# Kernel tuning notes

Measured on AMD Instinct MI355X. Metric: run time of the kernel, lower is better.

## Reference

```python
import jax, jax.numpy as jnp
import numpy as np

SEQ_LEN = 16384
IN_DIM = 2048
STATE_DIM = 2048


def setup_inputs() -> dict:
    key = jax.random.key(0)
    k_xs, k_lam, k_win, k_c, k_d = jax.random.split(key, 5)
    xs = jax.random.normal(k_xs, (SEQ_LEN, IN_DIM), dtype=jnp.float32)
    # diagonal state-transition values in (0, 1) for stability
    lam = jax.random.uniform(k_lam, (STATE_DIM,), dtype=jnp.float32)
    w_in = jax.random.normal(k_win, (STATE_DIM, IN_DIM), dtype=jnp.float32) / np.float32(np.sqrt(IN_DIM))
    c_out = jax.random.normal(k_c, (IN_DIM, STATE_DIM), dtype=jnp.float32) / np.float32(np.sqrt(STATE_DIM))
    d_skip = jax.random.normal(k_d, (IN_DIM,), dtype=jnp.float32)
    return {"xs": xs, "lam": lam, "w_in": w_in, "c_out": c_out, "d_skip": d_skip}


def _ssm_cell(a, b):
    # Faithful replication of BaseSSMLayer.ssm_cell (including its use of
    # matrix_pow_i * matrix_pow_i for the first component, exactly as in source).
    matrix_pow_i, bx_i = a
    matrix_pow_j, bx_j = b
    return (matrix_pow_i * matrix_pow_i, matrix_pow_j * bx_i + bx_j)


def reference(xs, lam, w_in, c_out, d_skip):
    seq_len = xs.shape[0]
    # discretize: broadcast diagonal lambda over the sequence -> [L, N]
    lambda_elements = jnp.broadcast_to(lam, (seq_len, lam.shape[0]))
    # preprocess_inputs: vmap(w_in @ x) == xs @ w_in.T  -> [L, N]
    w_in_xs = jnp.einsum('li,ni->ln', xs, w_in)
    _, hs = jax.lax.associative_scan(_ssm_cell, (lambda_elements, w_in_xs))
    # postprocess: y_t = C h_t + D * x_t  -> [L, in_dim]
    return jnp.einsum('ln,on->lo', hs, c_out) + xs * d_skip
```

## Files before the change

### kernel.cpp

```cpp
#include <hip/hip_runtime.h>

#define SEQ   16384
#define DIM   2048
#define CHUNK 128
#define NCHUNK (SEQ / CHUNK)

typedef __attribute__((ext_vector_type(8))) short  short8;
typedef __attribute__((ext_vector_type(4))) short  short4v;
typedef __attribute__((ext_vector_type(4))) float  floatx4;

static __device__ __forceinline__ float bf2f(short s) {
    return __uint_as_float(((unsigned)(unsigned short)s) << 16);
}
static __device__ __forceinline__ short f2bf(float f) {
    unsigned u = __float_as_uint(f);
    u += 0x7fff + ((u >> 16) & 1);
    return (short)(u >> 16);
}

__global__ void cast_kernel(const float* __restrict__ in, short* __restrict__ out, int n4) {
    int i = blockIdx.x * blockDim.x + threadIdx.x;
    if (i >= n4) return;
    float4 v = ((const float4*)in)[i];
    short4v s;
    s.x = f2bf(v.x); s.y = f2bf(v.y); s.z = f2bf(v.z); s.w = f2bf(v.w);
    ((short4v*)out)[i] = s;
}


#define BAR   __builtin_amdgcn_s_barrier()
#define PRIO1 __builtin_amdgcn_s_setprio(1)
#define PRIO0 __builtin_amdgcn_s_setprio(0)
#define VMC6  asm volatile("s_waitcnt vmcnt(6)" ::: "memory")
#define VMC0  asm volatile("s_waitcnt vmcnt(0)" ::: "memory")

#define STAGE_A(b, h, t) do { \
    const short* _s = Abase + (size_t)(h) * 128 * K + (size_t)(t) * 64; \
    __builtin_amdgcn_global_load_lds(_s + gOff0, &As[b][h][c0 * 8], 16, 0, 0); \
    __builtin_amdgcn_global_load_lds(_s + gOff1, &As[b][h][c1 * 8], 16, 0, 0); \
} while (0)
#define STAGE_B(b, h, t) do { \
    const short* _s = Bbase + (size_t)(h) * 128 * K + (size_t)(t) * 64; \
    __builtin_amdgcn_global_load_lds(_s + gOff0, &Bs[b][h][c0 * 8], 16, 0, 0); \
    __builtin_amdgcn_global_load_lds(_s + gOff1, &Bs[b][h][c1 * 8], 16, 0, 0); \
} while (0)

#define LDA(b, mh) \
    _Pragma("unroll") \
    for (int mi = 0; mi < 4; mi++) { \
        _Pragma("unroll") \
        for (int ks = 0; ks < 2; ks++) \
            aV[mi][ks] = *(const short8*)&As[b][mh][(arow + mi * 16) * 64 + \
                                                    ((((ks << 2) | quad) ^ sx) << 3)]; \
    }
#define LDB(dst, b, nh) \
    _Pragma("unroll") \
    for (int ni = 0; ni < 2; ni++) { \
        _Pragma("unroll") \
        for (int ks = 0; ks < 2; ks++) \
            dst[ni][ks] = *(const short8*)&Bs[b][nh][(brow + ni * 16) * 64 + \
                                                     ((((ks << 2) | quad) ^ sx) << 3)]; \
    }
#define MMA(mh, nh, bR) \
    _Pragma("unroll") \
    for (int mi = 0; mi < 4; mi++) { \
        _Pragma("unroll") \
        for (int ni = 0; ni < 2; ni++) { \
            acc[mh][nh][mi][ni] = __builtin_amdgcn_mfma_f32_16x16x32_bf16( \
                aV[mi][0], bR[ni][0], acc[mh][nh][mi][ni], 0, 0, 0); \
            acc[mh][nh][mi][ni] = __builtin_amdgcn_mfma_f32_16x16x32_bf16( \
                aV[mi][1], bR[ni][1], acc[mh][nh][mi][ni], 0, 0, 0); \
        } \
    }

template<int FUSE>
__global__ __launch_bounds__(512, 2)
void gemm_bt(const short* __restrict__ A, const short* __restrict__ B,
             short* __restrict__ Cbf, float* __restrict__ Cf,
             const float* __restrict__ xs, const float* __restrict__ dskip)
{
    constexpr int K  = DIM;
    constexpr int NT = K / 64;

    __shared__ alignas(16) short As[2][2][128 * 64];
    __shared__ alignas(16) short Bs[2][2][128 * 64];

    const int tid = threadIdx.x;
    const int m0  = blockIdx.y * 256;
    const int n0  = blockIdx.x * 256;

    const int lane = tid & 63;
    const int wv   = tid >> 6;
    const int wrow = wv >> 2;
    const int wcol = wv & 3;
    const int l16  = lane & 15;
    const int quad = lane >> 4;
    const int sx   = l16 & 7;
    const int arow = wrow * 64 + l16;
    const int brow = wcol * 32 + l16;

    const int c0 = tid, c1 = tid + 512;
    const int r0 = c0 >> 3, r1 = c1 >> 3;
    const size_t gOff0 = (size_t)r0 * K + (size_t)((((c0 & 7) ^ (r0 & 7))) * 8);
    const size_t gOff1 = (size_t)r1 * K + (size_t)((((c1 & 7) ^ (r1 & 7))) * 8);
    const short* Abase = A + (size_t)m0 * K;
    const short* Bbase = B + (size_t)n0 * K;

    short8  aV[4][2], bA[2][2], bB[2][2];
    floatx4 acc[2][2][4][2] = {};

    STAGE_A(0, 0, 0); STAGE_B(0, 0, 0); STAGE_B(0, 1, 0); STAGE_A(0, 1, 0);
    STAGE_A(1, 0, 1); STAGE_B(1, 0, 1); STAGE_B(1, 1, 1);
    VMC6;
    BAR;

    for (int i = 0; i < NT / 2; ++i) {
        const int t1 = 2 * i + 1;
        const int t2 = (2 * i + 2) & (NT - 1);
        const int t3 = (2 * i + 3) & (NT - 1);

        LDA(0, 0); LDB(bA, 0, 0); STAGE_A(1, 1, t1);
        PRIO1; MMA(0, 0, bA); PRIO0;
        BAR;
        LDB(bB, 0, 1); STAGE_A(0, 0, t2);
        PRIO1; MMA(0, 1, bB); PRIO0;
        BAR;
        LDA(0, 1); STAGE_B(0, 0, t2);
        PRIO1; MMA(1, 0, bA); PRIO0;
        BAR;
        STAGE_B(0, 1, t2);
        PRIO1; MMA(1, 1, bB); PRIO0;
        VMC6;
        BAR;
        LDA(1, 0); LDB(bA, 1, 0); STAGE_A(0, 1, t2);
        PRIO1; MMA(0, 0, bA); PRIO0;
        BAR;
        LDB(bB, 1, 1); STAGE_A(1, 0, t3);
        PRIO1; MMA(0, 1, bB); PRIO0;
        BAR;
        LDA(1, 1); STAGE_B(1, 0, t3);
        PRIO1; MMA(1, 0, bA); PRIO0;
        BAR;
        STAGE_B(1, 1, t3);
        PRIO1; MMA(1, 1, bB); PRIO0;
        VMC6;
        BAR;
    }
    VMC0;

    if (FUSE == 0) {
        #pragma unroll
        for (int mh = 0; mh < 2; mh++)
        #pragma unroll
        for (int mi = 0; mi < 4; mi++) {
            const int rb = m0 + wrow * 64 + mh * 128 + mi * 16 + quad * 4;
            #pragma unroll
            for (int nh = 0; nh < 2; nh++)
            #pragma unroll
            for (int ni = 0; ni < 2; ni++) {
                const int cc = n0 + wcol * 32 + nh * 128 + ni * 16 + l16;
                #pragma unroll
                for (int r = 0; r < 4; r++)
                    Cbf[(size_t)(rb + r) * DIM + cc] = f2bf(acc[mh][nh][mi][ni][r]);
            }
        }
    } else {
        float dsk[2][2];
        #pragma unroll
        for (int nh = 0; nh < 2; nh++)
        #pragma unroll
        for (int ni = 0; ni < 2; ni++)
            dsk[nh][ni] = dskip[n0 + wcol * 32 + nh * 128 + ni * 16 + l16];
        #pragma unroll
        for (int mh = 0; mh < 2; mh++)
        #pragma unroll
        for (int mi = 0; mi < 4; mi++) {
            const int rb = m0 + wrow * 64 + mh * 128 + mi * 16 + quad * 4;
            #pragma unroll
            for (int nh = 0; nh < 2; nh++)
            #pragma unroll
            for (int ni = 0; ni < 2; ni++) {
                const int cc = n0 + wcol * 32 + nh * 128 + ni * 16 + l16;
                #pragma unroll
                for (int r = 0; r < 4; r++) {
                    size_t idx = (size_t)(rb + r) * DIM + cc;
                    Cf[idx] = acc[mh][nh][mi][ni][r] + xs[idx] * dsk[nh][ni];
                }
            }
        }
    }
}

__global__ void scan_pass1(const short* __restrict__ bx, const float* __restrict__ lam,
                           float* __restrict__ blockLast)
{
    int q     = blockIdx.x * 256 + threadIdx.x;
    int n     = q * 4;
    int chunk = blockIdx.y;
    float4 lm = *(const float4*)&lam[n];
    const uint2* p = (const uint2*)(bx + (size_t)chunk * CHUNK * DIM) + q;
    float h0 = 0.f, h1 = 0.f, h2 = 0.f, h3 = 0.f;
    #pragma unroll 16
    for (int i = 0; i < CHUNK; i++) {
        uint2 v = p[(size_t)i * (DIM / 4)];
        h0 = fmaf(lm.x, h0, bf2f((short)(v.x & 0xffffu)));
        h1 = fmaf(lm.y, h1, bf2f((short)(v.x >> 16)));
        h2 = fmaf(lm.z, h2, bf2f((short)(v.y & 0xffffu)));
        h3 = fmaf(lm.w, h3, bf2f((short)(v.y >> 16)));
    }
    float4 o; o.x = h0; o.y = h1; o.z = h2; o.w = h3;
    *(float4*)&blockLast[(size_t)chunk * DIM + n] = o;
}

__global__ void scan_pass2(float* __restrict__ blockLast, const float* __restrict__ lam)
{
    int q = blockIdx.x * 256 + threadIdx.x;
    int n = q * 4;
    float4 lm = *(const float4*)&lam[n];
    float p0 = lm.x, p1 = lm.y, p2 = lm.z, p3 = lm.w;
    #pragma unroll
    for (int i = 0; i < 7; i++) { p0 *= p0; p1 *= p1; p2 *= p2; p3 *= p3; }
    float c0 = 0.f, c1 = 0.f, c2 = 0.f, c3 = 0.f;
    for (int c = 0; c < NCHUNK; c++) {
        float4* qp = (float4*)&blockLast[(size_t)c * DIM + n];
        float4 t = *qp;
        float4 w; w.x = c0; w.y = c1; w.z = c2; w.w = c3;
        *qp = w;
        c0 = fmaf(p0, c0, t.x);
        c1 = fmaf(p1, c1, t.y);
        c2 = fmaf(p2, c2, t.z);
        c3 = fmaf(p3, c3, t.w);
    }
}

__global__ void scan_pass3(short* __restrict__ bxh, const float* __restrict__ lam,
                           const float* __restrict__ carry)
{
    int q     = blockIdx.x * 256 + threadIdx.x;
    int n     = q * 4;
    int chunk = blockIdx.y;
    float4 lm = *(const float4*)&lam[n];
    float4 cv = *(const float4*)&carry[(size_t)chunk * DIM + n];
    float h0 = cv.x, h1 = cv.y, h2 = cv.z, h3 = cv.w;
    uint2* p = (uint2*)(bxh + (size_t)chunk * CHUNK * DIM) + q;
    #pragma unroll 16
    for (int i = 0; i < CHUNK; i++) {
        uint2 v = p[(size_t)i * (DIM / 4)];
        h0 = fmaf(lm.x, h0, bf2f((short)(v.x & 0xffffu)));
        h1 = fmaf(lm.y, h1, bf2f((short)(v.x >> 16)));
        h2 = fmaf(lm.z, h2, bf2f((short)(v.y & 0xffffu)));
        h3 = fmaf(lm.w, h3, bf2f((short)(v.y >> 16)));
        uint2 o;
        o.x = (unsigned)(unsigned short)f2bf(h0) | ((unsigned)(unsigned short)f2bf(h1) << 16);
        o.y = (unsigned)(unsigned short)f2bf(h2) | ((unsigned)(unsigned short)f2bf(h3) << 16);
        p[(size_t)i * (DIM / 4)] = o;
    }
}

extern "C" void kernel_launch(void* const* d_in, const int* in_sizes, int n_in,
                              void* d_out, int out_size, void* d_ws, size_t ws_size,
                              hipStream_t stream)
{
    const float* xs    = (const float*)d_in[0];
    const float* lam   = (const float*)d_in[1];
    const float* w_in  = (const float*)d_in[2];
    const float* c_out = (const float*)d_in[3];
    const float* dskip = (const float*)d_in[4];
    float* out = (float*)d_out;

    char*  ws    = (char*)d_ws;
    short* bxh   = (short*)ws;
    short* w_bf  = (short*)(ws + (size_t)64 * 1024 * 1024);
    short* c_bf  = (short*)(ws + (size_t)72 * 1024 * 1024);
    short* xs_bf = (short*)d_out;
    float* blkl  = (float*)((char*)d_out + (size_t)100 * 1024 * 1024);

    cast_kernel<<<SEQ * DIM / 4 / 256, 256, 0, stream>>>(xs, xs_bf, SEQ * DIM / 4);
    cast_kernel<<<DIM * DIM / 4 / 256, 256, 0, stream>>>(w_in, w_bf, DIM * DIM / 4);
    cast_kernel<<<DIM * DIM / 4 / 256, 256, 0, stream>>>(c_out, c_bf, DIM * DIM / 4);

    dim3 ggrid(DIM / 256, SEQ / 256);
    gemm_bt<0><<<ggrid, 512, 0, stream>>>(xs_bf, w_bf, bxh, nullptr, nullptr, nullptr);

    dim3 sgrid(DIM / 1024, NCHUNK);
    scan_pass1<<<sgrid, 256, 0, stream>>>(bxh, lam, blkl);
    scan_pass2<<<DIM / 1024, 256, 0, stream>>>(blkl, lam);
    scan_pass3<<<sgrid, 256, 0, stream>>>(bxh, lam, blkl);

    gemm_bt<1><<<ggrid, 512, 0, stream>>>(bxh, c_bf, nullptr, out, xs, dskip);
}
```

Baseline: 567.6 us.

## Double-buffer GEMM register fragments and widen scan carry pass parallelism

Restructures the GEMM main loop so LDS-to-register loads for the next sub-tile are issued into a second register set while MFMAs run on the current one, with lgkmcnt/vmcnt waits reordered and a prologue preload added. The aim is to hide LDS read latency behind matrix math. It raises register pressure, which could hurt occupancy at launch bounds of 512 threads with 2 blocks. Separately, the sequential carry-propagation pass now uses one state element per thread across 8 blocks instead of float4 per thread across 2 blocks, giving more parallelism to a latency-bound serial loop.

```diff
diff --git a/kernel.cpp b/kernel.cpp
--- a/kernel.cpp
+++ b/kernel.cpp
@@ -31,7 +31,8 @@
 #define BAR   __builtin_amdgcn_s_barrier()
 #define PRIO1 __builtin_amdgcn_s_setprio(1)
 #define PRIO0 __builtin_amdgcn_s_setprio(0)
-#define VMC6  asm volatile("s_waitcnt vmcnt(6)" ::: "memory")
+#define LGKM0 asm volatile("s_waitcnt lgkmcnt(0)" ::: "memory")
+#define VMC4  asm volatile("s_waitcnt vmcnt(4)" ::: "memory")
 #define VMC0  asm volatile("s_waitcnt vmcnt(0)" ::: "memory")
 
 #define STAGE_A(b, h, t) do { \
@@ -45,15 +46,15 @@
     __builtin_amdgcn_global_load_lds(_s + gOff1, &Bs[b][h][c1 * 8], 16, 0, 0); \
 } while (0)
 
-#define LDA(b, mh) \
+#define LDA_(dst, b, mh) \
     _Pragma("unroll") \
     for (int mi = 0; mi < 4; mi++) { \
         _Pragma("unroll") \
         for (int ks = 0; ks < 2; ks++) \
-            aV[mi][ks] = *(const short8*)&As[b][mh][(arow + mi * 16) * 64 + \
-                                                    ((((ks << 2) | quad) ^ sx) << 3)]; \
-    }
-#define LDB(dst, b, nh) \
+            dst[mi][ks] = *(const short8*)&As[b][mh][(arow + mi * 16) * 64 + \
+                                                     ((((ks << 2) | quad) ^ sx) << 3)]; \
+    }
+#define LDB_(dst, b, nh) \
     _Pragma("unroll") \
     for (int ni = 0; ni < 2; ni++) { \
         _Pragma("unroll") \
@@ -61,15 +62,15 @@
             dst[ni][ks] = *(const short8*)&Bs[b][nh][(brow + ni * 16) * 64 + \
                                                      ((((ks << 2) | quad) ^ sx) << 3)]; \
     }
-#define MMA(mh, nh, bR) \
+#define MMA(mh, nh, Aset, Bset) \
     _Pragma("unroll") \
     for (int mi = 0; mi < 4; mi++) { \
         _Pragma("unroll") \
         for (int ni = 0; ni < 2; ni++) { \
             acc[mh][nh][mi][ni] = __builtin_amdgcn_mfma_f32_16x16x32_bf16( \
-                aV[mi][0], bR[ni][0], acc[mh][nh][mi][ni], 0, 0, 0); \
+                Aset[mi][0], Bset[ni][0], acc[mh][nh][mi][ni], 0, 0, 0); \
             acc[mh][nh][mi][ni] = __builtin_amdgcn_mfma_f32_16x16x32_bf16( \
-                aV[mi][1], bR[ni][1], acc[mh][nh][mi][ni], 0, 0, 0); \
+                Aset[mi][1], Bset[ni][1], acc[mh][nh][mi][ni], 0, 0, 0); \
         } \
     }
 
@@ -106,44 +107,54 @@
     const short* Abase = A + (size_t)m0 * K;
     const short* Bbase = B + (size_t)n0 * K;
 
-    short8  aV[4][2], bA[2][2], bB[2][2];
+    short8  A0[4][2], A1[4][2], B0[2][2], B1[2][2];
     floatx4 acc[2][2][4][2] = {};
 
-    STAGE_A(0, 0, 0); STAGE_B(0, 0, 0); STAGE_B(0, 1, 0); STAGE_A(0, 1, 0);
-    STAGE_A(1, 0, 1); STAGE_B(1, 0, 1); STAGE_B(1, 1, 1);
-    VMC6;
+    STAGE_A(0, 0, 0); STAGE_B(0, 0, 0); STAGE_A(0, 1, 0); STAGE_B(0, 1, 0);
+    STAGE_A(1, 0, 1); STAGE_B(1, 0, 1);
+    VMC4;
     BAR;
+    LDA_(A0, 0, 0); LDB_(B0, 0, 0);
+    STAGE_A(1, 1, 1); STAGE_B(1, 1, 1);
 
     for (int i = 0; i < NT / 2; ++i) {
-        const int t1 = 2 * i + 1;
-        const int t2 = (2 * i + 2) & (NT - 1);
-        const int t3 = (2 * i + 3) & (NT - 1);
-
-        LDA(0, 0); LDB(bA, 0, 0); STAGE_A(1, 1, t1);
-        PRIO1; MMA(0, 0, bA); PRIO0;
-        BAR;
-        LDB(bB, 0, 1); STAGE_A(0, 0, t2);
-        PRIO1; MMA(0, 1, bB); PRIO0;
-        BAR;
-        LDA(0, 1); STAGE_B(0, 0, t2);
-        PRIO1; MMA(1, 0, bA); PRIO0;
-        BAR;
-        STAGE_B(0, 1, t2);
-        PRIO1; MMA(1, 1, bB); PRIO0;
-        VMC6;
-        BAR;
-        LDA(1, 0); LDB(bA, 1, 0); STAGE_A(0, 1, t2);
-        PRIO1; MMA(0, 0, bA); PRIO0;
-        BAR;
-        LDB(bB, 1, 1); STAGE_A(1, 0, t3);
-        PRIO1; MMA(0, 1, bB); PRIO0;
-        BAR;
-        LDA(1, 1); STAGE_B(1, 0, t3);
-        PRIO1; MMA(1, 0, bA); PRIO0;
-        BAR;
-        STAGE_B(1, 1, t3);
-        PRIO1; MMA(1, 1, bB); PRIO0;
-        VMC6;
+        const int tE = (2 * i + 2) & (NT - 1);
+        const int tO = (2 * i + 3) & (NT - 1);
+
+        LGKM0;
+        STAGE_A(0, 0, tE);
+        LDB_(B1, 0, 1); LDA_(A1, 0, 1);
+        PRIO1; MMA(0, 0, A0, B0); PRIO0;
+        BAR;
+        STAGE_B(0, 0, tE);
+        PRIO1; MMA(0, 1, A0, B1); PRIO0;
+        BAR;
+        LGKM0;
+        VMC4;
+        STAGE_A(0, 1, tE);
+        PRIO1; MMA(1, 0, A1, B0); PRIO0;
+        LDA_(A0, 1, 0); LDB_(B0, 1, 0);
+        BAR;
+        STAGE_B(0, 1, tE);
+        PRIO1; MMA(1, 1, A1, B1); PRIO0;
+        BAR;
+
+        LGKM0;
+        STAGE_A(1, 0, tO);
+        LDB_(B1, 1, 1); LDA_(A1, 1, 1);
+        PRIO1; MMA(0, 0, A0, B0); PRIO0;
+        BAR;
+        STAGE_B(1, 0, tO);
+        PRIO1; MMA(0, 1, A0, B1); PRIO0;
+        BAR;
+        LGKM0;
+        VMC4;
+        STAGE_A(1, 1, tO);
+        PRIO1; MMA(1, 0, A1, B0); PRIO0;
+        LDA_(A0, 0, 0); LDB_(B0, 0, 0);
+        BAR;
+        STAGE_B(1, 1, tO);
+        PRIO1; MMA(1, 1, A1, B1); PRIO0;
         BAR;
     }
     VMC0;
@@ -214,22 +225,17 @@
 
 __global__ void scan_pass2(float* __restrict__ blockLast, const float* __restrict__ lam)
 {
-    int q = blockIdx.x * 256 + threadIdx.x;
-    int n = q * 4;
-    float4 lm = *(const float4*)&lam[n];
-    float p0 = lm.x, p1 = lm.y, p2 = lm.z, p3 = lm.w;
+    int n = blockIdx.x * 256 + threadIdx.x;
+    float lm = lam[n];
+    float p = lm;
     #pragma unroll
-    for (int i = 0; i < 7; i++) { p0 *= p0; p1 *= p1; p2 *= p2; p3 *= p3; }
-    float c0 = 0.f, c1 = 0.f, c2 = 0.f, c3 = 0.f;
+    for (int i = 0; i < 7; i++) p = p * p;
+    float carry = 0.f;
+    #pragma unroll 4
     for (int c = 0; c < NCHUNK; c++) {
-        float4* qp = (float4*)&blockLast[(size_t)c * DIM + n];
-        float4 t = *qp;
-        float4 w; w.x = c0; w.y = c1; w.z = c2; w.w = c3;
-        *qp = w;
-        c0 = fmaf(p0, c0, t.x);
-        c1 = fmaf(p1, c1, t.y);
-        c2 = fmaf(p2, c2, t.z);
-        c3 = fmaf(p3, c3, t.w);
+        float t = blockLast[(size_t)c * DIM + n];
+        blockLast[(size_t)c * DIM + n] = carry;
+        carry = fmaf(p, carry, t);
     }
 }
 
@@ -284,7 +290,7 @@
 
     dim3 sgrid(DIM / 1024, NCHUNK);
     scan_pass1<<<sgrid, 256, 0, stream>>>(bxh, lam, blkl);
-    scan_pass2<<<DIM / 1024, 256, 0, stream>>>(blkl, lam);
+    scan_pass2<<<DIM / 256, 256, 0, stream>>>(blkl, lam);
     scan_pass3<<<sgrid, 256, 0, stream>>>(bxh, lam, blkl);
 
     gemm_bt<1><<<ggrid, 512, 0, stream>>>(bxh, c_bf, nullptr, out, xs, dskip);
```

New measurement: 571.6 us. Within noise of the previous version (+0.7%).
